# Optimization experiments

Measured on AMD Instinct MI355X. Metric: run time of the kernel, lower is better.

Reference implementation:

```python
import jax, jax.numpy as jnp
import numpy as np

B, S, EMB = 2, 2048, 4096
NHEADS, KVHEADS, HEAD_D = 32, 8, 128
SPLITS = (NHEADS * HEAD_D, KVHEADS * HEAD_D, KVHEADS * HEAD_D)  # 4096, 1024, 1024


def setup_inputs() -> dict:
    key = jax.random.key(0)
    k1, k2, k3 = jax.random.split(key, 3)
    q = jax.random.normal(k1, (B, S, EMB), dtype=jnp.float32)
    # nn.Linear weights, torch layout [out_features, in_features], std=0.02 init
    w_qkv = jax.random.normal(k2, (sum(SPLITS), EMB), dtype=jnp.float32) * 0.02
    w_dense = jax.random.normal(k3, (EMB, NHEADS * HEAD_D), dtype=jnp.float32) * 0.02
    return {"q": q, "w_qkv": w_qkv, "w_dense": w_dense}


def reference(q, w_qkv, w_dense):
    # Self-attention path of PagedMultiHeadAttention (no cache), causal mask.
    Bq, Sq, _ = q.shape
    qkv = q @ w_qkv.T                                  # [B, S, 6144]
    qs, ks, vs = jnp.split(qkv, np.cumsum(SPLITS)[:-1], axis=-1)
    G = NHEADS // KVHEADS                              # GQA expansion = 4
    # queries grouped per kv-head: [B, S, KVH, G, D]
    qh = qs.reshape(Bq, Sq, KVHEADS, G, HEAD_D)
    kh = ks.reshape(Bq, Sq, KVHEADS, HEAD_D)
    vh = vs.reshape(Bq, Sq, KVHEADS, HEAD_D)
    scale = 1.0 / jnp.sqrt(jnp.float32(HEAD_D))
    scores = jnp.einsum("bskgd,btkd->bkgst", qh, kh) * scale  # [B,KVH,G,S,S]
    causal = jnp.tril(jnp.ones((Sq, Sq), dtype=bool))
    scores = jnp.where(causal, scores, jnp.finfo(scores.dtype).min)
    probs = jax.nn.softmax(scores, axis=-1)
    attn = jnp.einsum("bkgst,btkd->bskgd", probs, vh)  # [B,S,KVH,G,D]
    attn = attn.reshape(Bq, Sq, NHEADS * HEAD_D)
    return attn @ w_dense.T                            # [B, S, EMB]
```

## Files before the change

### kernel.cpp

```cpp
#include <hip/hip_runtime.h>
#include <hip/hip_bf16.h>

typedef __bf16 bf16x8 __attribute__((ext_vector_type(8)));
typedef __bf16 bf16x4 __attribute__((ext_vector_type(4)));
typedef float  f32x4  __attribute__((ext_vector_type(4)));

typedef __attribute__((address_space(3))) void lds_vp;
typedef const __attribute__((address_space(1))) void gbl_vp;

__global__ void cast_f32_bf16(const float* __restrict__ src, __bf16* __restrict__ dst, int n8) {
    int i = blockIdx.x * 256 + threadIdx.x;
    if (i >= n8) return;
    const float4* s = (const float4*)src;
    float4 a = s[2 * i], b = s[2 * i + 1];
    bf16x8 o;
    o[0] = (__bf16)a.x; o[1] = (__bf16)a.y; o[2] = (__bf16)a.z; o[3] = (__bf16)a.w;
    o[4] = (__bf16)b.x; o[5] = (__bf16)b.y; o[6] = (__bf16)b.z; o[7] = (__bf16)b.w;
    ((bf16x8*)dst)[i] = o;
}


__device__ __forceinline__ void stage_half(const __bf16* __restrict__ g, int K, int kt,
                                           __bf16* lds_tile, int h, int w, int l) {
#pragma unroll
    for (int j = 0; j < 2; ++j) {
        const int rih = (j * 8 + w) * 8 + (l >> 3);
        const __bf16* src = g + (size_t)(h * 128 + rih) * K + kt * 64 + (((l & 7) ^ (l >> 3)) << 3);
        __bf16* dst = lds_tile + h * 8192 + (j * 8 + w) * 512;
        __builtin_amdgcn_global_load_lds((gbl_vp*)src, (lds_vp*)dst, 16, 0, 0);
    }
}

__device__ __forceinline__ bf16x8 lds_frag(const __bf16* base, int row, int kb) {
    return *(const bf16x8*)((const char*)base + row * 128 + (kb ^ ((row & 7) << 4)));
}

template <int OUT_BF16>
__global__ __launch_bounds__(512, 2)
void gemm256(const __bf16* __restrict__ A, const __bf16* __restrict__ Bm,
             void* __restrict__ Cout, int M, int N, int K) {
    __shared__ __bf16 As[2][256 * 64];
    __shared__ __bf16 Bs[2][256 * 64];
    const int tid = threadIdx.x;
    const int lane = tid & 63, wid = tid >> 6;
    const int g = lane >> 4, lq = lane & 15;
    const int wm = wid >> 2, wn = wid & 3;
    const size_t brow = (size_t)blockIdx.y * 256, bcol = (size_t)blockIdx.x * 256;
    const __bf16* Ag = A + brow * K;
    const __bf16* Bg = Bm + bcol * K;
    const int nkt = K >> 6;

    f32x4 acc[8][4] = {};

    stage_half(Ag, K, 0, &As[0][0], 0, wid, lane);
    stage_half(Bg, K, 0, &Bs[0][0], 0, wid, lane);
    stage_half(Ag, K, 0, &As[0][0], 1, wid, lane);
    stage_half(Bg, K, 0, &Bs[0][0], 1, wid, lane);

    const int arow0 = wm * 128 + lq;
    const int brow0 = wn * 64 + lq;

    for (int t = 0; t < nkt; ++t) {
        const int cur = t & 1;
        const __bf16* SA = &As[cur][0];
        const __bf16* SB = &Bs[cur][0];
        __bf16* DA = &As[cur ^ 1][0];
        __bf16* DB = &Bs[cur ^ 1][0];
        const int ts = t + 1;
        const bool dostage = (ts < nkt);
        bf16x8 bfr[4][2];

        if (dostage) {
            stage_half(Bg, K, ts, DB, 0, wid, lane);
            stage_half(Bg, K, ts, DB, 1, wid, lane);
        }
        __builtin_amdgcn_sched_barrier(0);
        if (dostage) asm volatile("s_waitcnt vmcnt(4)" ::: "memory");
        else         asm volatile("s_waitcnt vmcnt(0)" ::: "memory");
        __builtin_amdgcn_s_barrier();
        __builtin_amdgcn_sched_barrier(0);
#pragma unroll
        for (int n = 0; n < 4; ++n)
#pragma unroll
            for (int kk = 0; kk < 2; ++kk)
                bfr[n][kk] = lds_frag(SB, brow0 + n * 16, kk * 64 + g * 16);
        {
            bf16x8 afr[2][2];
#pragma unroll
            for (int mm = 0; mm < 2; ++mm)
#pragma unroll
                for (int kk = 0; kk < 2; ++kk)
                    afr[mm][kk] = lds_frag(SA, arow0 + mm * 16, kk * 64 + g * 16);
            __builtin_amdgcn_s_setprio(1);
#pragma unroll
            for (int kk = 0; kk < 2; ++kk)
#pragma unroll
                for (int n = 0; n < 4; ++n)
#pragma unroll
                    for (int mm = 0; mm < 2; ++mm)
                        acc[mm][n] = __builtin_amdgcn_mfma_f32_16x16x32_bf16(afr[mm][kk], bfr[n][kk], acc[mm][n], 0, 0, 0);
            __builtin_amdgcn_s_setprio(0);
        }
        __builtin_amdgcn_sched_barrier(0);
        __builtin_amdgcn_s_barrier();
        __builtin_amdgcn_sched_barrier(0);

#pragma unroll
        for (int q = 1; q < 4; ++q) {
            bf16x8 afr[2][2];
#pragma unroll
            for (int mm = 0; mm < 2; ++mm)
#pragma unroll
                for (int kk = 0; kk < 2; ++kk)
                    afr[mm][kk] = lds_frag(SA, arow0 + (q * 2 + mm) * 16, kk * 64 + g * 16);
            if (dostage && q == 1) {
                stage_half(Ag, K, ts, DA, 0, wid, lane);
                stage_half(Ag, K, ts, DA, 1, wid, lane);
            }
            __builtin_amdgcn_sched_barrier(0);
            __builtin_amdgcn_s_barrier();
            __builtin_amdgcn_sched_barrier(0);
            __builtin_amdgcn_s_setprio(1);
#pragma unroll
            for (int kk = 0; kk < 2; ++kk)
#pragma unroll
                for (int n = 0; n < 4; ++n)
#pragma unroll
                    for (int mm = 0; mm < 2; ++mm)
                        acc[q * 2 + mm][n] = __builtin_amdgcn_mfma_f32_16x16x32_bf16(afr[mm][kk], bfr[n][kk], acc[q * 2 + mm][n], 0, 0, 0);
            __builtin_amdgcn_s_setprio(0);
            __builtin_amdgcn_sched_barrier(0);
            __builtin_amdgcn_s_barrier();
            __builtin_amdgcn_sched_barrier(0);
        }
    }

#pragma unroll
    for (int m = 0; m < 8; ++m) {
#pragma unroll
        for (int r = 0; r < 4; ++r) {
            size_t row = brow + wm * 128 + m * 16 + g * 4 + r;
#pragma unroll
            for (int n = 0; n < 4; ++n) {
                size_t col = bcol + wn * 64 + n * 16 + lq;
                float v = acc[m][n][r];
                if (OUT_BF16) ((__bf16*)Cout)[row * N + col] = (__bf16)v;
                else          ((float*)Cout)[row * N + col] = v;
            }
        }
    }
}

__global__ __launch_bounds__(256)
void transpose_v(const __bf16* __restrict__ qkv, __bf16* __restrict__ vt) {
    constexpr int S = 2048, QKVN = 6144;
    __shared__ __bf16 tile[64][72];
    const int tt = blockIdx.x;
    const int yz = blockIdx.y;
    const int dh = yz & 1, bkh = yz >> 1;
    const int b = bkh >> 3, kh = bkh & 7;
    const int tid = threadIdx.x;
#pragma unroll
    for (int i = 0; i < 2; ++i) {
        int flat = i * 2048 + tid * 8;
        int r = flat >> 6, c0 = flat & 63;
        const __bf16* src = qkv + ((size_t)b * S + tt * 64 + r) * QKVN + 5120 + kh * 128 + dh * 64 + c0;
        *(bf16x8*)&tile[r][c0] = *(const bf16x8*)src;
    }
    __syncthreads();
#pragma unroll
    for (int i = 0; i < 2; ++i) {
        int flat = i * 2048 + tid * 8;
        int d = flat >> 6, t0 = flat & 63;
        bf16x8 pk;
#pragma unroll
        for (int e = 0; e < 8; ++e) pk[e] = tile[t0 + e][d];
        __bf16* dst = vt + ((size_t)(b * 8 + kh) * 128 + dh * 64 + d) * S + tt * 64 + t0;
        *(bf16x8*)dst = pk;
    }
}

__global__ __launch_bounds__(256, 2)
void attn_kernel(const __bf16* __restrict__ qkv, const __bf16* __restrict__ vt,
                 __bf16* __restrict__ outb) {
    constexpr int S = 2048, D = 128, QKVN = 6144;
    const int p = blockIdx.x;
    const int kh = p & 7;
    const int j = p >> 3;
    const int qt = 15 - (j >> 3);
    const int b  = (j >> 2) & 1;
    const int g4 = j & 3;
    const int h  = kh * 4 + g4;
    const int tid = threadIdx.x, lane = tid & 63, w = tid >> 6;
    const int g = lane >> 4, lq = lane & 15;

    __shared__ __bf16 Ks[64 * 128];
    __shared__ __bf16 Vs[128 * 64];
    __shared__ char   PsRaw[4][2][16 * 152];

    const int wqmin = qt * 128 + w * 32;
    const int qg0 = wqmin + lq;
    const int qg1 = qg0 + 16;

    const __bf16* qrow = qkv + ((size_t)(b * S) + wqmin + lq) * QKVN + h * D;
    bf16x8 qf0[4], qf1[4];
#pragma unroll
    for (int ks = 0; ks < 4; ++ks) {
        qf0[ks] = *(const bf16x8*)(qrow + ks * 32 + g * 8);
        qf1[ks] = *(const bf16x8*)(qrow + (size_t)16 * QKVN + ks * 32 + g * 8);
    }

    const char* kbase = (const char*)qkv + ((size_t)(b * S) * QKVN + 4096 + kh * D) * 2;
    const char* vbase = (const char*)vt + ((size_t)(b * 8 + kh) * D * S) * 2;

    f32x4 acc0[8] = {}, acc1[8] = {};
    float m0 = -1e30f, l0 = 0.f, m1 = -1e30f, l1 = 0.f;
    const float scale2 = 0.12753102494f;

    const int krow0 = tid >> 4;
    const int kcolb = (tid & 15) * 16;
    const int vrow0 = tid >> 3;
    const int vcolb = (tid & 7) * 16;

    const int ktmax = 2 * qt + 1;
    int4 pk[4], pv[4];
#pragma unroll
    for (int is = 0; is < 4; ++is) {
        pk[is] = *(const int4*)(kbase + (size_t)(is * 16 + krow0) * QKVN * 2 + kcolb);
        pv[is] = *(const int4*)(vbase + (size_t)(is * 32 + vrow0) * S * 2 + vcolb);
    }

    char* ps0 = &PsRaw[w][0][0];
    char* ps1 = &PsRaw[w][1][0];

    for (int kt = 0; kt <= ktmax; ++kt) {
        __builtin_amdgcn_s_barrier();
#pragma unroll
        for (int is = 0; is < 4; ++is) {
            int row = is * 16 + krow0;
            *(int4*)((char*)Ks + row * 256 + (kcolb ^ ((row & 15) << 4))) = pk[is];
            int d = is * 32 + vrow0;
            *(int4*)((char*)Vs + d * 128 + (vcolb ^ ((d & 7) << 4))) = pv[is];
        }
        if (kt < ktmax) {
#pragma unroll
            for (int is = 0; is < 4; ++is) {
                pk[is] = *(const int4*)(kbase + (size_t)((kt + 1) * 64 + is * 16 + krow0) * QKVN * 2 + kcolb);
                pv[is] = *(const int4*)(vbase + ((size_t)(is * 32 + vrow0) * S + (kt + 1) * 64) * 2 + vcolb);
            }
        }
        __builtin_amdgcn_sched_barrier(0);
        asm volatile("s_waitcnt lgkmcnt(0)" ::: "memory");
        __builtin_amdgcn_sched_barrier(0);
        __builtin_amdgcn_s_barrier();
        __builtin_amdgcn_sched_barrier(0);

        if (kt * 64 <= wqmin + 31) {
            f32x4 sc0[4], sc1[4];
            __builtin_amdgcn_s_setprio(1);
#pragma unroll
            for (int tb = 0; tb < 4; ++tb) {
                f32x4 s0 = {0.f, 0.f, 0.f, 0.f}, s1 = {0.f, 0.f, 0.f, 0.f};
                const int trow = tb * 16 + lq;
                const int rsw = (trow & 15) << 4;
#pragma unroll
                for (int ks = 0; ks < 4; ++ks) {
                    bf16x8 kf = *(const bf16x8*)((const char*)Ks + trow * 256 + ((ks * 64 + g * 16) ^ rsw));
                    s0 = __builtin_amdgcn_mfma_f32_16x16x32_bf16(kf, qf0[ks], s0, 0, 0, 0);
                    s1 = __builtin_amdgcn_mfma_f32_16x16x32_bf16(kf, qf1[ks], s1, 0, 0, 0);
                }
                sc0[tb] = s0; sc1[tb] = s1;
            }
            __builtin_amdgcn_s_setprio(0);

#pragma unroll
            for (int f = 0; f < 2; ++f) {
                f32x4* sc = f ? sc1 : sc0;
                float& m_r = f ? m1 : m0;
                float& l_p = f ? l1 : l0;
                f32x4* acc = f ? acc1 : acc0;
                char* ps = f ? ps1 : ps0;
                const int qg = f ? qg1 : qg0;
                const bool domask = (kt * 64 + 63 > qg - lq);

                float pr[16];
                float rowmax = -1e30f;
#pragma unroll
                for (int tb = 0; tb < 4; ++tb)
#pragma unroll
                    for (int r = 0; r < 4; ++r) {
                        float sv = sc[tb][r] * scale2;
                        if (domask) {
                            int tg = kt * 64 + tb * 16 + g * 4 + r;
                            sv = (tg <= qg) ? sv : -1e30f;
                        }
                        pr[tb * 4 + r] = sv;
                        rowmax = fmaxf(rowmax, sv);
                    }
                rowmax = fmaxf(rowmax, __shfl_xor(rowmax, 16));
                rowmax = fmaxf(rowmax, __shfl_xor(rowmax, 32));
                if (!__all(rowmax - m_r <= 11.0f)) {
                    float m_new = fmaxf(m_r, rowmax);
                    float alpha = exp2f(m_r - m_new);
                    l_p *= alpha;
#pragma unroll
                    for (int r = 0; r < 4; ++r) {
                        float ar = __shfl(alpha, g * 4 + r);
#pragma unroll
                        for (int nb = 0; nb < 8; ++nb) acc[nb][r] *= ar;
                    }
                    m_r = m_new;
                }
                float lsum = 0.f;
#pragma unroll
                for (int i = 0; i < 16; ++i) {
                    float e = exp2f(pr[i] - m_r);
                    pr[i] = e;
                    lsum += e;
                }
                l_p += lsum;
#pragma unroll
                for (int tb = 0; tb < 4; ++tb) {
                    bf16x4 pkv;
#pragma unroll
                    for (int r = 0; r < 4; ++r) pkv[r] = (__bf16)pr[tb * 4 + r];
                    *(bf16x4*)(ps + lq * 152 + tb * 32 + g * 8) = pkv;
                }
            }

            __builtin_amdgcn_s_setprio(1);
#pragma unroll
            for (int ks = 0; ks < 2; ++ks) {
                bf16x8 pa0 = *(const bf16x8*)(ps0 + lq * 152 + ks * 64 + g * 16);
                bf16x8 pa1 = *(const bf16x8*)(ps1 + lq * 152 + ks * 64 + g * 16);
#pragma unroll
                for (int nb = 0; nb < 8; ++nb) {
                    int d = nb * 16 + lq;
                    bf16x8 vf = *(const bf16x8*)((const char*)Vs + d * 128 + ((ks * 64 + g * 16) ^ ((d & 7) << 4)));
                    acc0[nb] = __builtin_amdgcn_mfma_f32_16x16x32_bf16(pa0, vf, acc0[nb], 0, 0, 0);
                    acc1[nb] = __builtin_amdgcn_mfma_f32_16x16x32_bf16(pa1, vf, acc1[nb], 0, 0, 0);
                }
            }
            __builtin_amdgcn_s_setprio(0);
        }
        __builtin_amdgcn_sched_barrier(0);
    }

    l0 += __shfl_xor(l0, 16); l0 += __shfl_xor(l0, 32);
    l1 += __shfl_xor(l1, 16); l1 += __shfl_xor(l1, 32);
    float rl0 = 1.f / l0, rl1 = 1.f / l1;
#pragma unroll
    for (int r = 0; r < 4; ++r) {
        float rr0 = __shfl(rl0, g * 4 + r);
        float rr1 = __shfl(rl1, g * 4 + r);
        size_t row0 = (size_t)(b * S) + wqmin + g * 4 + r;
        __bf16* orow0 = outb + row0 * 4096 + h * D;
        __bf16* orow1 = orow0 + (size_t)16 * 4096;
#pragma unroll
        for (int nb = 0; nb < 8; ++nb) {
            orow0[nb * 16 + lq] = (__bf16)(acc0[nb][r] * rr0);
            orow1[nb * 16 + lq] = (__bf16)(acc1[nb][r] * rr1);
        }
    }
}

extern "C" void kernel_launch(void* const* d_in, const int* in_sizes, int n_in,
                              void* d_out, int out_size, void* d_ws, size_t ws_size,
                              hipStream_t stream) {
    (void)in_sizes; (void)n_in; (void)out_size; (void)ws_size;
    const float* q       = (const float*)d_in[0];
    const float* w_qkv   = (const float*)d_in[1];
    const float* w_dense = (const float*)d_in[2];
    float* out = (float*)d_out;
    char* ws = (char*)d_ws;

    __bf16* qbf      = (__bf16*)(ws);
    __bf16* wqkvbf   = (__bf16*)(ws + 33554432ULL);
    __bf16* wdensebf = (__bf16*)(ws + 83886080ULL);
    __bf16* qkvbf    = (__bf16*)(ws + 117440512ULL);
    __bf16* vtbf     = (__bf16*)(ws + 167772160ULL);
    __bf16* attnbf   = (__bf16*)(ws + 176160768ULL);

    cast_f32_bf16<<<8192, 256, 0, stream>>>(q, qbf, 2097152);
    cast_f32_bf16<<<12288, 256, 0, stream>>>(w_qkv, wqkvbf, 3145728);
    cast_f32_bf16<<<8192, 256, 0, stream>>>(w_dense, wdensebf, 2097152);

    gemm256<1><<<dim3(24, 16), 512, 0, stream>>>(qbf, wqkvbf, (void*)qkvbf, 4096, 6144, 4096);
    transpose_v<<<dim3(32, 32), 256, 0, stream>>>(qkvbf, vtbf);
    attn_kernel<<<1024, 256, 0, stream>>>(qkvbf, vtbf, attnbf);
    gemm256<0><<<dim3(16, 16), 512, 0, stream>>>(attnbf, wdensebf, (void*)out, 4096, 4096, 4096);
}
```

Baseline: 728.2 us.

## Restructure GEMM main loop to one barrier per k-tile with prefetched LDS fragments

The bf16 GEMM main loop now waits for global loads and syncs once at the top of each k-tile, then issues all four next-tile A/B stages together. Previously it used several barriers per iteration and staged A and B at different points. LDS fragment reads for later row groups are issued ahead of the MFMA blocks and gated with partial lgkmcnt waits, so LDS latency overlaps matrix math. The cost is more live fragment registers under a tight launch bound, and the full vmcnt(0) wait at the top of each tile may expose global-load latency.

```diff
diff --git a/kernel.cpp b/kernel.cpp
--- a/kernel.cpp
+++ b/kernel.cpp
@@ -18,7 +18,6 @@
     o[4] = (__bf16)b.x; o[5] = (__bf16)b.y; o[6] = (__bf16)b.z; o[7] = (__bf16)b.w;
     ((bf16x8*)dst)[i] = o;
 }
-
 
 __device__ __forceinline__ void stage_half(const __bf16* __restrict__ g, int K, int kt,
                                            __bf16* lds_tile, int h, int w, int l) {
@@ -66,73 +65,98 @@
         const __bf16* SB = &Bs[cur][0];
         __bf16* DA = &As[cur ^ 1][0];
         __bf16* DB = &Bs[cur ^ 1][0];
-        const int ts = t + 1;
-        const bool dostage = (ts < nkt);
-        bf16x8 bfr[4][2];
+        const bool dostage = (t + 1 < nkt);
+
+        asm volatile("s_waitcnt vmcnt(0)" ::: "memory");
+        __builtin_amdgcn_s_barrier();
+        __builtin_amdgcn_sched_barrier(0);
 
         if (dostage) {
-            stage_half(Bg, K, ts, DB, 0, wid, lane);
-            stage_half(Bg, K, ts, DB, 1, wid, lane);
-        }
-        __builtin_amdgcn_sched_barrier(0);
-        if (dostage) asm volatile("s_waitcnt vmcnt(4)" ::: "memory");
-        else         asm volatile("s_waitcnt vmcnt(0)" ::: "memory");
-        __builtin_amdgcn_s_barrier();
-        __builtin_amdgcn_sched_barrier(0);
+            stage_half(Ag, K, t + 1, DA, 0, wid, lane);
+            stage_half(Bg, K, t + 1, DB, 0, wid, lane);
+            stage_half(Ag, K, t + 1, DA, 1, wid, lane);
+            stage_half(Bg, K, t + 1, DB, 1, wid, lane);
+        }
+        __builtin_amdgcn_sched_barrier(0);
+
+        bf16x8 bfr[4][2], afr0[2][2], afr1[2][2], afr2[2][2], afr3[2][2];
 #pragma unroll
         for (int n = 0; n < 4; ++n)
 #pragma unroll
             for (int kk = 0; kk < 2; ++kk)
                 bfr[n][kk] = lds_frag(SB, brow0 + n * 16, kk * 64 + g * 16);
-        {
-            bf16x8 afr[2][2];
-#pragma unroll
-            for (int mm = 0; mm < 2; ++mm)
-#pragma unroll
-                for (int kk = 0; kk < 2; ++kk)
-                    afr[mm][kk] = lds_frag(SA, arow0 + mm * 16, kk * 64 + g * 16);
-            __builtin_amdgcn_s_setprio(1);
+#pragma unroll
+        for (int mm = 0; mm < 2; ++mm)
+#pragma unroll
+            for (int kk = 0; kk < 2; ++kk) {
+                afr0[mm][kk] = lds_frag(SA, arow0 + mm * 16, kk * 64 + g * 16);
+                afr1[mm][kk] = lds_frag(SA, arow0 + (2 + mm) * 16, kk * 64 + g * 16);
+            }
+        __builtin_amdgcn_sched_barrier(0);
+
+        asm volatile("s_waitcnt lgkmcnt(4)" ::: "memory");
+        __builtin_amdgcn_sched_barrier(0);
+        __builtin_amdgcn_s_setprio(1);
+#pragma unroll
+        for (int kk = 0; kk < 2; ++kk)
+#pragma unroll
+            for (int n = 0; n < 4; ++n)
+#pragma unroll
+                for (int mm = 0; mm < 2; ++mm)
+                    acc[mm][n] = __builtin_amdgcn_mfma_f32_16x16x32_bf16(afr0[mm][kk], bfr[n][kk], acc[mm][n], 0, 0, 0);
+        __builtin_amdgcn_s_setprio(0);
+        __builtin_amdgcn_sched_barrier(0);
+#pragma unroll
+        for (int mm = 0; mm < 2; ++mm)
 #pragma unroll
             for (int kk = 0; kk < 2; ++kk)
-#pragma unroll
-                for (int n = 0; n < 4; ++n)
-#pragma unroll
-                    for (int mm = 0; mm < 2; ++mm)
-                        acc[mm][n] = __builtin_amdgcn_mfma_f32_16x16x32_bf16(afr[mm][kk], bfr[n][kk], acc[mm][n], 0, 0, 0);
-            __builtin_amdgcn_s_setprio(0);
-        }
-        __builtin_amdgcn_sched_barrier(0);
-        __builtin_amdgcn_s_barrier();
-        __builtin_amdgcn_sched_barrier(0);
-
-#pragma unroll
-        for (int q = 1; q < 4; ++q) {
-            bf16x8 afr[2][2];
-#pragma unroll
-            for (int mm = 0; mm < 2; ++mm)
-#pragma unroll
-                for (int kk = 0; kk < 2; ++kk)
-                    afr[mm][kk] = lds_frag(SA, arow0 + (q * 2 + mm) * 16, kk * 64 + g * 16);
-            if (dostage && q == 1) {
-                stage_half(Ag, K, ts, DA, 0, wid, lane);
-                stage_half(Ag, K, ts, DA, 1, wid, lane);
-            }
-            __builtin_amdgcn_sched_barrier(0);
-            __builtin_amdgcn_s_barrier();
-            __builtin_amdgcn_sched_barrier(0);
-            __builtin_amdgcn_s_setprio(1);
+                afr2[mm][kk] = lds_frag(SA, arow0 + (4 + mm) * 16, kk * 64 + g * 16);
+        __builtin_amdgcn_sched_barrier(0);
+
+        asm volatile("s_waitcnt lgkmcnt(4)" ::: "memory");
+        __builtin_amdgcn_sched_barrier(0);
+        __builtin_amdgcn_s_setprio(1);
+#pragma unroll
+        for (int kk = 0; kk < 2; ++kk)
+#pragma unroll
+            for (int n = 0; n < 4; ++n)
+#pragma unroll
+                for (int mm = 0; mm < 2; ++mm)
+                    acc[2 + mm][n] = __builtin_amdgcn_mfma_f32_16x16x32_bf16(afr1[mm][kk], bfr[n][kk], acc[2 + mm][n], 0, 0, 0);
+        __builtin_amdgcn_s_setprio(0);
+        __builtin_amdgcn_sched_barrier(0);
+#pragma unroll
+        for (int mm = 0; mm < 2; ++mm)
 #pragma unroll
             for (int kk = 0; kk < 2; ++kk)
-#pragma unroll
-                for (int n = 0; n < 4; ++n)
-#pragma unroll
-                    for (int mm = 0; mm < 2; ++mm)
-                        acc[q * 2 + mm][n] = __builtin_amdgcn_mfma_f32_16x16x32_bf16(afr[mm][kk], bfr[n][kk], acc[q * 2 + mm][n], 0, 0, 0);
-            __builtin_amdgcn_s_setprio(0);
-            __builtin_amdgcn_sched_barrier(0);
-            __builtin_amdgcn_s_barrier();
-            __builtin_amdgcn_sched_barrier(0);
-        }
+                afr3[mm][kk] = lds_frag(SA, arow0 + (6 + mm) * 16, kk * 64 + g * 16);
+        __builtin_amdgcn_sched_barrier(0);
+
+        asm volatile("s_waitcnt lgkmcnt(4)" ::: "memory");
+        __builtin_amdgcn_sched_barrier(0);
+        __builtin_amdgcn_s_setprio(1);
+#pragma unroll
+        for (int kk = 0; kk < 2; ++kk)
+#pragma unroll
+            for (int n = 0; n < 4; ++n)
+#pragma unroll
+                for (int mm = 0; mm < 2; ++mm)
+                    acc[4 + mm][n] = __builtin_amdgcn_mfma_f32_16x16x32_bf16(afr2[mm][kk], bfr[n][kk], acc[4 + mm][n], 0, 0, 0);
+        __builtin_amdgcn_s_setprio(0);
+        __builtin_amdgcn_sched_barrier(0);
+
+        asm volatile("s_waitcnt lgkmcnt(0)" ::: "memory");
+        __builtin_amdgcn_sched_barrier(0);
+        __builtin_amdgcn_s_setprio(1);
+#pragma unroll
+        for (int kk = 0; kk < 2; ++kk)
+#pragma unroll
+            for (int n = 0; n < 4; ++n)
+#pragma unroll
+                for (int mm = 0; mm < 2; ++mm)
+                    acc[6 + mm][n] = __builtin_amdgcn_mfma_f32_16x16x32_bf16(afr3[mm][kk], bfr[n][kk], acc[6 + mm][n], 0, 0, 0);
+        __builtin_amdgcn_s_setprio(0);
+        __builtin_amdgcn_sched_barrier(0);
     }
 
 #pragma unroll
```

Result: faster. 712.1 us (-2.2%).
